# Optimization experiments

Measured on AMD Instinct MI355X. Metric: run time of the kernel, lower is better.

The kernel has to match this reference:

```python
import jax, jax.numpy as jnp
import numpy as np

N, D, H = 524288, 64, 256


def setup_inputs() -> dict:
    key = jax.random.key(0)
    k1, k2, k3 = jax.random.split(key, 3)
    X = jax.random.normal(k1, (N, D), dtype=jnp.float32)
    centers = jax.random.normal(k2, (H, D), dtype=jnp.float32)
    w = jax.random.normal(k3, (1, H), dtype=jnp.float32) / np.sqrt(H)
    b = jnp.zeros((1,), dtype=jnp.float32)
    return {"X": X, "centers": centers, "w": w, "b": b}


def reference(X, centers, w, b):
    # RBF feature map: phi[n, h] = exp(-||X[n] - centers[h]||^2)
    # Squared euclidean distance via the expanded form to avoid the
    # [N, H, D] broadcast intermediate the naive torch version builds.
    x2 = jnp.sum(X * X, axis=-1, keepdims=True)           # [N, 1]
    c2 = jnp.sum(centers * centers, axis=-1)               # [H]
    xc = jnp.einsum('nd,hd->nh', X, centers)               # [N, H]
    d2 = jnp.maximum(x2 - 2.0 * xc + c2[None, :], 0.0)     # [N, H]
    feats = jnp.exp(-d2)                                   # gaussian kernel
    # Linear head: nn.Linear(hidden_dim, 1)
    return feats @ w.T + b                                 # [N, 1]
```

## Files before the change

kernel.cpp:

```cpp
#include <hip/hip_runtime.h>

#define NROWS 524288
#define DDIM  64
#define HCENT 256
#define GRID  512
#define CPB   4

typedef short bf16x8 __attribute__((ext_vector_type(8)));
typedef float f32x4  __attribute__((ext_vector_type(4)));

#define LOG2E 1.4426950408889634f
#define K2L   2.8853900817779268f
#define BIASF 80.0f

__device__ __forceinline__ float fast_exp2(float x) {
#if __has_builtin(__builtin_amdgcn_exp2f)
  return __builtin_amdgcn_exp2f(x);
#else
  return exp2f(x);
#endif
}

__global__ __attribute__((amdgpu_flat_work_group_size(512, 512),
                          amdgpu_waves_per_eu(4, 4)))
void rbf_main(const float* __restrict__ X,
              const float* __restrict__ bptr,
              const float* __restrict__ centers,
              const float* __restrict__ w,
              float* __restrict__ out) {
  __shared__ int4 BH[16 * 2 * 64];
  __shared__ int4 BL[16 * 2 * 64];
  __shared__ float2 CWs[HCENT];

  const int tid  = threadIdx.x;
  const int wave = tid >> 6;
  const int lane = tid & 63;
  const int q    = lane >> 4;
  const int c    = lane & 15;

  float c2a[2] = {0.f, 0.f};
#pragma unroll
  for (int i = 0; i < 4; ++i) {
    int pair = wave * 4 + i;
    int ct = pair >> 1;
    int kc = pair & 1;
    const float* src = centers + (ct * 16 + c) * DDIM + kc * 32 + q * 8;
    float4 f0 = reinterpret_cast<const float4*>(src)[0];
    float4 f1 = reinterpret_cast<const float4*>(src)[1];
    float xs[8] = {f0.x, f0.y, f0.z, f0.w, f1.x, f1.y, f1.z, f1.w};
    float ss = 0.f;
    int hp[4], lp[4];
#pragma unroll
    for (int p = 0; p < 4; ++p) {
      float x0 = xs[2 * p], x1 = xs[2 * p + 1];
      ss = fmaf(x0, x0, ss);
      ss = fmaf(x1, x1, ss);
      unsigned u0 = __float_as_uint(x0);
      unsigned u1 = __float_as_uint(x1);
      float l0 = x0 - __uint_as_float(u0 & 0xFFFF0000u);
      float l1 = x1 - __uint_as_float(u1 & 0xFFFF0000u);
      hp[p] = (int)((u1 & 0xFFFF0000u) | (u0 >> 16));
      lp[p] = (int)((__float_as_uint(l1) & 0xFFFF0000u) | (__float_as_uint(l0) >> 16));
    }
    c2a[i >> 1] += ss;
    int idx = pair * 64 + lane;
    BH[idx] = make_int4(hp[0], hp[1], hp[2], hp[3]);
    BL[idx] = make_int4(lp[0], lp[1], lp[2], lp[3]);
  }
#pragma unroll
  for (int t = 0; t < 2; ++t) {
    int ct = wave * 2 + t;
    float s2 = c2a[t];
    s2 += __shfl_xor(s2, 16, 64);
    s2 += __shfl_xor(s2, 32, 64);
    if (q == 0) {
      int h = ct * 16 + c;
      CWs[h] = make_float2(-fmaf(s2, LOG2E, BIASF), w[h]);
    }
  }

  float bval = bptr[0];

  __syncthreads();

  const bf16x8* BHv = reinterpret_cast<const bf16x8*>(BH);
  const bf16x8* BLv = reinterpret_cast<const bf16x8*>(BL);

  f32x4 raw[2][4];

  {
    int rowbase0 = (blockIdx.x * CPB + 0) * 256 + wave * 32;
#pragma unroll
    for (int rt = 0; rt < 2; ++rt) {
      const float* rp = X + (rowbase0 + rt * 16 + c) * DDIM + q * 8;
      raw[rt][0] = reinterpret_cast<const f32x4*>(rp)[0];
      raw[rt][1] = reinterpret_cast<const f32x4*>(rp)[1];
      raw[rt][2] = reinterpret_cast<const f32x4*>(rp + 32)[0];
      raw[rt][3] = reinterpret_cast<const f32x4*>(rp + 32)[1];
    }
  }

#pragma unroll 1
  for (int s = 0; s < CPB; ++s) {
    int rowbase = (blockIdx.x * CPB + s) * 256 + wave * 32;

    bf16x8 ah[2][2], al[2][2];
    float x2p[2];
#pragma unroll
    for (int rt = 0; rt < 2; ++rt) {
      float part = 0.f;
#pragma unroll
      for (int kc = 0; kc < 2; ++kc) {
        f32x4 f0 = raw[rt][kc * 2];
        f32x4 f1 = raw[rt][kc * 2 + 1];
        float xs[8] = {f0.x, f0.y, f0.z, f0.w, f1.x, f1.y, f1.z, f1.w};
        union { int i[4]; bf16x8 v; } uh, ul;
#pragma unroll
        for (int p = 0; p < 4; ++p) {
          float x0 = xs[2 * p], x1 = xs[2 * p + 1];
          part = fmaf(x0, x0, part);
          part = fmaf(x1, x1, part);
          unsigned u0 = __float_as_uint(x0);
          unsigned u1 = __float_as_uint(x1);
          float l0 = x0 - __uint_as_float(u0 & 0xFFFF0000u);
          float l1 = x1 - __uint_as_float(u1 & 0xFFFF0000u);
          uh.i[p] = (int)((u1 & 0xFFFF0000u) | (u0 >> 16));
          ul.i[p] = (int)((__float_as_uint(l1) & 0xFFFF0000u) | (__float_as_uint(l0) >> 16));
        }
        ah[rt][kc] = uh.v;
        al[rt][kc] = ul.v;
      }
      x2p[rt] = part;
    }

    if (s + 1 < CPB) {
      int rbn = (blockIdx.x * CPB + s + 1) * 256 + wave * 32;
#pragma unroll
      for (int rt = 0; rt < 2; ++rt) {
        const float* rp = X + (rbn + rt * 16 + c) * DDIM + q * 8;
        raw[rt][0] = reinterpret_cast<const f32x4*>(rp)[0];
        raw[rt][1] = reinterpret_cast<const f32x4*>(rp)[1];
        raw[rt][2] = reinterpret_cast<const f32x4*>(rp + 32)[0];
        raw[rt][3] = reinterpret_cast<const f32x4*>(rp + 32)[1];
      }
    }

    float psum[2][4] = {{0.f, 0.f, 0.f, 0.f}, {0.f, 0.f, 0.f, 0.f}};
#pragma unroll 2
    for (int ct = 0; ct < 16; ++ct) {
      int idx = ct * 128 + lane;
      bf16x8 bh0 = BHv[idx], bh1 = BHv[idx + 64];
      bf16x8 bl0 = BLv[idx], bl1 = BLv[idx + 64];
      float2 mw = CWs[ct * 16 + c];
#pragma unroll
      for (int rt = 0; rt < 2; ++rt) {
        f32x4 acc = {0.f, 0.f, 0.f, 0.f};
        acc = __builtin_amdgcn_mfma_f32_16x16x32_bf16(ah[rt][0], bh0, acc, 0, 0, 0);
        acc = __builtin_amdgcn_mfma_f32_16x16x32_bf16(ah[rt][1], bh1, acc, 0, 0, 0);
        acc = __builtin_amdgcn_mfma_f32_16x16x32_bf16(al[rt][0], bh0, acc, 0, 0, 0);
        acc = __builtin_amdgcn_mfma_f32_16x16x32_bf16(al[rt][1], bh1, acc, 0, 0, 0);
        acc = __builtin_amdgcn_mfma_f32_16x16x32_bf16(ah[rt][0], bl0, acc, 0, 0, 0);
        acc = __builtin_amdgcn_mfma_f32_16x16x32_bf16(ah[rt][1], bl1, acc, 0, 0, 0);
#pragma unroll
        for (int r = 0; r < 4; ++r) {
          float e = fast_exp2(fmaf(acc[r], K2L, mw.x));
          psum[rt][r] = fmaf(e, mw.y, psum[rt][r]);
        }
      }
    }

#pragma unroll
    for (int rt = 0; rt < 2; ++rt) {
      float part = x2p[rt];
      part += __shfl_xor(part, 16, 64);
      part += __shfl_xor(part, 32, 64);
#pragma unroll
      for (int r = 0; r < 4; ++r) {
        float v = psum[rt][r];
        v += __shfl_xor(v, 1, 64);
        v += __shfl_xor(v, 2, 64);
        v += __shfl_xor(v, 4, 64);
        v += __shfl_xor(v, 8, 64);
        float x2row = __shfl(part, q * 4 + r, 64);
        float rowf = fast_exp2(fmaf(-LOG2E, x2row, BIASF));
        psum[rt][r] = fmaf(v, rowf, bval);
      }
      if (c == 0) {
        f32x4 o = {psum[rt][0], psum[rt][1], psum[rt][2], psum[rt][3]};
        *reinterpret_cast<f32x4*>(out + rowbase + rt * 16 + q * 4) = o;
      }
    }
  }
}

extern "C" void kernel_launch(void* const* d_in, const int* in_sizes, int n_in,
                              void* d_out, int out_size, void* d_ws, size_t ws_size,
                              hipStream_t stream) {
  const float* X       = (const float*)d_in[0];
  const float* centers = (const float*)d_in[1];
  const float* w       = (const float*)d_in[2];
  const float* b       = (const float*)d_in[3];
  float* out = (float*)d_out;

  rbf_main<<<GRID, 512, 0, stream>>>(X, b, centers, w, out);
}
```

Measured before the change: 225.7 us.

## Use 1024-thread blocks, drop X register prefetch, use v_perm for bf16 packing

Doubles the block size to 1024 threads (16 waves) with launch bounds targeting higher occupancy, so each wave prepares one center tile and each block iteration covers 512 rows over 2 iterations instead of 4. Removes the cross-iteration software prefetch of X rows and loads them at the start of each iteration, relying on more resident waves to hide latency instead. Replaces shift/mask bf16 packing with a single byte-permute instruction and stops unrolling the inner center loop to cut register pressure. Loses explicit load/compute overlap and may hit register limits under the new launch bounds.

```diff
diff --git a/kernel.cpp b/kernel.cpp
--- a/kernel.cpp
+++ b/kernel.cpp
@@ -1,10 +1,9 @@
 #include <hip/hip_runtime.h>
 
-#define NROWS 524288
 #define DDIM  64
 #define HCENT 256
 #define GRID  512
-#define CPB   4
+#define CPB   2
 
 typedef short bf16x8 __attribute__((ext_vector_type(8)));
 typedef float f32x4  __attribute__((ext_vector_type(4)));
@@ -21,8 +20,7 @@
 #endif
 }
 
-__global__ __attribute__((amdgpu_flat_work_group_size(512, 512),
-                          amdgpu_waves_per_eu(4, 4)))
+__global__ __launch_bounds__(1024, 8)
 void rbf_main(const float* __restrict__ X,
               const float* __restrict__ bptr,
               const float* __restrict__ centers,
@@ -38,43 +36,38 @@
   const int q    = lane >> 4;
   const int c    = lane & 15;
 
-  float c2a[2] = {0.f, 0.f};
+  float c2s = 0.f;
 #pragma unroll
-  for (int i = 0; i < 4; ++i) {
-    int pair = wave * 4 + i;
-    int ct = pair >> 1;
-    int kc = pair & 1;
+  for (int kc = 0; kc < 2; ++kc) {
+    int ct = wave;
     const float* src = centers + (ct * 16 + c) * DDIM + kc * 32 + q * 8;
-    float4 f0 = reinterpret_cast<const float4*>(src)[0];
-    float4 f1 = reinterpret_cast<const float4*>(src)[1];
+    f32x4 f0 = reinterpret_cast<const f32x4*>(src)[0];
+    f32x4 f1 = reinterpret_cast<const f32x4*>(src)[1];
     float xs[8] = {f0.x, f0.y, f0.z, f0.w, f1.x, f1.y, f1.z, f1.w};
-    float ss = 0.f;
     int hp[4], lp[4];
 #pragma unroll
     for (int p = 0; p < 4; ++p) {
       float x0 = xs[2 * p], x1 = xs[2 * p + 1];
-      ss = fmaf(x0, x0, ss);
-      ss = fmaf(x1, x1, ss);
+      c2s = fmaf(x0, x0, c2s);
+      c2s = fmaf(x1, x1, c2s);
       unsigned u0 = __float_as_uint(x0);
       unsigned u1 = __float_as_uint(x1);
       float l0 = x0 - __uint_as_float(u0 & 0xFFFF0000u);
       float l1 = x1 - __uint_as_float(u1 & 0xFFFF0000u);
-      hp[p] = (int)((u1 & 0xFFFF0000u) | (u0 >> 16));
-      lp[p] = (int)((__float_as_uint(l1) & 0xFFFF0000u) | (__float_as_uint(l0) >> 16));
+      hp[p] = (int)__builtin_amdgcn_perm(u1, u0, 0x07060302u);
+      lp[p] = (int)__builtin_amdgcn_perm(__float_as_uint(l1), __float_as_uint(l0),
+                                         0x07060302u);
     }
-    c2a[i >> 1] += ss;
-    int idx = pair * 64 + lane;
+    int idx = (ct * 2 + kc) * 64 + lane;
     BH[idx] = make_int4(hp[0], hp[1], hp[2], hp[3]);
     BL[idx] = make_int4(lp[0], lp[1], lp[2], lp[3]);
   }
-#pragma unroll
-  for (int t = 0; t < 2; ++t) {
-    int ct = wave * 2 + t;
-    float s2 = c2a[t];
+  {
+    float s2 = c2s;
     s2 += __shfl_xor(s2, 16, 64);
     s2 += __shfl_xor(s2, 32, 64);
     if (q == 0) {
-      int h = ct * 16 + c;
+      int h = wave * 16 + c;
       CWs[h] = make_float2(-fmaf(s2, LOG2E, BIASF), w[h]);
     }
   }
@@ -86,23 +79,23 @@
   const bf16x8* BHv = reinterpret_cast<const bf16x8*>(BH);
   const bf16x8* BLv = reinterpret_cast<const bf16x8*>(BL);
 
-  f32x4 raw[2][4];
-
-  {
-    int rowbase0 = (blockIdx.x * CPB + 0) * 256 + wave * 32;
-#pragma unroll
-    for (int rt = 0; rt < 2; ++rt) {
-      const float* rp = X + (rowbase0 + rt * 16 + c) * DDIM + q * 8;
-      raw[rt][0] = reinterpret_cast<const f32x4*>(rp)[0];
-      raw[rt][1] = reinterpret_cast<const f32x4*>(rp)[1];
-      raw[rt][2] = reinterpret_cast<const f32x4*>(rp + 32)[0];
-      raw[rt][3] = reinterpret_cast<const f32x4*>(rp + 32)[1];
-    }
-  }
-
 #pragma unroll 1
   for (int s = 0; s < CPB; ++s) {
-    int rowbase = (blockIdx.x * CPB + s) * 256 + wave * 32;
+    int rowbase = (blockIdx.x * CPB + s) * 512 + wave * 32;
+
+    f32x4 r0, r1, r2, r3, r4, r5, r6, r7;
+    {
+      const float* rp0 = X + (rowbase + c) * DDIM + q * 8;
+      const float* rp1 = X + (rowbase + 16 + c) * DDIM + q * 8;
+      r0 = reinterpret_cast<const f32x4*>(rp0)[0];
+      r1 = reinterpret_cast<const f32x4*>(rp0)[1];
+      r2 = reinterpret_cast<const f32x4*>(rp0 + 32)[0];
+      r3 = reinterpret_cast<const f32x4*>(rp0 + 32)[1];
+      r4 = reinterpret_cast<const f32x4*>(rp1)[0];
+      r5 = reinterpret_cast<const f32x4*>(rp1)[1];
+      r6 = reinterpret_cast<const f32x4*>(rp1 + 32)[0];
+      r7 = reinterpret_cast<const f32x4*>(rp1 + 32)[1];
+    }
 
     bf16x8 ah[2][2], al[2][2];
     float x2p[2];
@@ -111,8 +104,8 @@
       float part = 0.f;
 #pragma unroll
       for (int kc = 0; kc < 2; ++kc) {
-        f32x4 f0 = raw[rt][kc * 2];
-        f32x4 f1 = raw[rt][kc * 2 + 1];
+        f32x4 f0 = (rt == 0) ? (kc == 0 ? r0 : r2) : (kc == 0 ? r4 : r6);
+        f32x4 f1 = (rt == 0) ? (kc == 0 ? r1 : r3) : (kc == 0 ? r5 : r7);
         float xs[8] = {f0.x, f0.y, f0.z, f0.w, f1.x, f1.y, f1.z, f1.w};
         union { int i[4]; bf16x8 v; } uh, ul;
 #pragma unroll
@@ -124,8 +117,9 @@
           unsigned u1 = __float_as_uint(x1);
           float l0 = x0 - __uint_as_float(u0 & 0xFFFF0000u);
           float l1 = x1 - __uint_as_float(u1 & 0xFFFF0000u);
-          uh.i[p] = (int)((u1 & 0xFFFF0000u) | (u0 >> 16));
-          ul.i[p] = (int)((__float_as_uint(l1) & 0xFFFF0000u) | (__float_as_uint(l0) >> 16));
+          uh.i[p] = (int)__builtin_amdgcn_perm(u1, u0, 0x07060302u);
+          ul.i[p] = (int)__builtin_amdgcn_perm(__float_as_uint(l1),
+                                               __float_as_uint(l0), 0x07060302u);
         }
         ah[rt][kc] = uh.v;
         al[rt][kc] = ul.v;
@@ -133,20 +127,8 @@
       x2p[rt] = part;
     }
 
-    if (s + 1 < CPB) {
-      int rbn = (blockIdx.x * CPB + s + 1) * 256 + wave * 32;
-#pragma unroll
-      for (int rt = 0; rt < 2; ++rt) {
-        const float* rp = X + (rbn + rt * 16 + c) * DDIM + q * 8;
-        raw[rt][0] = reinterpret_cast<const f32x4*>(rp)[0];
-        raw[rt][1] = reinterpret_cast<const f32x4*>(rp)[1];
-        raw[rt][2] = reinterpret_cast<const f32x4*>(rp + 32)[0];
-        raw[rt][3] = reinterpret_cast<const f32x4*>(rp + 32)[1];
-      }
-    }
-
     float psum[2][4] = {{0.f, 0.f, 0.f, 0.f}, {0.f, 0.f, 0.f, 0.f}};
-#pragma unroll 2
+#pragma unroll 1
     for (int ct = 0; ct < 16; ++ct) {
       int idx = ct * 128 + lane;
       bf16x8 bh0 = BHv[idx], bh1 = BHv[idx + 64];
@@ -202,5 +184,5 @@
   const float* b       = (const float*)d_in[3];
   float* out = (float*)d_out;
 
-  rbf_main<<<GRID, 512, 0, stream>>>(X, b, centers, w, out);
+  rbf_main<<<GRID, 1024, 0, stream>>>(X, b, centers, w, out);
 }
```

Measured after the change: 243.3 us. +7.8%, slower.
